# Optimization experiments

Measured on AMD Instinct MI355X. Metric: run time of the kernel, lower is better.

## Reference

```python
import math
import jax, jax.numpy as jnp
import numpy as np

H_CYCLES, L_CYCLES = 3, 2
STD = 0.02


def setup_inputs() -> dict:
    key = jax.random.key(0)
    ks = jax.random.split(key, 11)
    D, nh, mult, V, T, B = 512, 8, 64, 8192, 512, 4
    N = mult * D // nh
    def nrm(k, shape):
        return jax.random.normal(k, shape, jnp.float32) * STD
    return {
        "idx": jax.random.randint(ks[0], (B, T), 0, V),
        "embed_w": nrm(ks[1], (V, D)),
        "h_enc": nrm(ks[2], (nh, D, N)),
        "h_enc_v": nrm(ks[3], (nh, D, N)),
        "h_dec": nrm(ks[4], (nh * N, D)),
        "l_enc": nrm(ks[5], (nh, D, N)),
        "l_enc_v": nrm(ks[6], (nh, D, N)),
        "l_dec": nrm(ks[7], (nh * N, D)),
        "lm_head": nrm(ks[8], (D, V)),
        "h_init": nrm(ks[9], (D,)),
        "l_init": nrm(ks[10], (D,)),
    }


def _ln(x, eps=1e-5):
    # LayerNorm without affine params (elementwise_affine=False)
    m = jnp.mean(x, axis=-1, keepdims=True)
    v = jnp.var(x, axis=-1, keepdims=True)
    return (x - m) * jax.lax.rsqrt(v + eps)


def _rope_tables(T, N):
    # freqs with even-quantized exponent, angles wrapped mod 1 then scaled by 2*pi
    q = jnp.floor(jnp.arange(N, dtype=jnp.float32) / 2.0) * 2.0
    freqs = 1.0 / jnp.power(2.0 ** 16, q / N) / (2.0 * math.pi)
    phases = jnp.arange(T, dtype=jnp.float32)[:, None] * freqs[None, :]
    ang = (phases % 1.0) * (2.0 * math.pi)
    return jnp.cos(ang), jnp.sin(ang)  # each (T, N)


def _rope(v, cos, sin):
    # v: (B, nh, T, N); interleaved rotation as in torch stack/view trick
    v_rot = jnp.stack((-v[..., 1::2], v[..., ::2]), axis=-1).reshape(v.shape)
    return v * cos + v_rot * sin


def _attn(x_sparse, Vmat, cos, sin):
    # x_sparse: (B, nh, T, N); Vmat: (B, T, D)
    N = x_sparse.shape[-1]
    T = x_sparse.shape[-2]
    QR = _rope(x_sparse, cos, sin)
    scores = jnp.einsum('bhtn,bhsn->bhts', QR, QR) * (N ** -0.5)
    mask = jnp.tril(jnp.ones((T, T), dtype=bool), k=-1)  # strict lower triangle
    scores = jnp.where(mask, scores, 0.0)
    return jnp.einsum('bhts,bsd->bhtd', scores, Vmat)  # (B, nh, T, D)


def _block(x, inj, enc, enc_v, dec, cos, sin):
    # x, inj: (B, 1, T, D)
    B, _, T, D = x.shape
    nh, _, N = enc.shape
    xi = _ln(x + inj)[:, 0]  # (B, T, D)
    x_sparse = jax.nn.relu(jnp.einsum('btd,hdn->bhtn', xi, enc))
    yKV = _ln(_attn(x_sparse, xi, cos, sin))  # (B, nh, T, D)
    y_sparse = jax.nn.relu(jnp.einsum('bhtd,hdn->bhtn', yKV, enc_v))
    xy = (x_sparse * y_sparse).transpose(0, 2, 1, 3).reshape(B, 1, T, nh * N)
    y = _ln(xy @ dec)  # (B, 1, T, D)
    return _ln(x + y)


def reference(idx, embed_w, h_enc, h_enc_v, h_dec, l_enc, l_enc_v, l_dec,
              lm_head, h_init, l_init):
    B, T = idx.shape
    D = embed_w.shape[1]
    N = l_enc.shape[-1]
    cos, sin = _rope_tables(T, N)
    inp = _ln(embed_w[idx])[:, None]  # (B, 1, T, D)
    z_H = jnp.broadcast_to(h_init, (B, 1, T, D))
    z_L = jnp.broadcast_to(l_init, (B, 1, T, D))
    for h in range(H_CYCLES):
        for l in range(L_CYCLES):
            if not (h == H_CYCLES - 1 and l == L_CYCLES - 1):
                z_L = _block(z_L, z_H + inp, l_enc, l_enc_v, l_dec, cos, sin)
        if h < H_CYCLES - 1:
            z_H = _block(z_H, z_L, h_enc, h_enc_v, h_dec, cos, sin)
    z_L = _block(z_L, z_H + inp, l_enc, l_enc_v, l_dec, cos, sin)
    z_H = _block(z_H, z_L, h_enc, h_enc_v, h_dec, cos, sin)
    logits = z_H[:, 0] @ lm_head  # (B, T, vocab)
    return logits
```

## Files before the change

### kernel.cpp

```cpp
#include <hip/hip_runtime.h>

typedef _Float16 f16;
typedef __attribute__((ext_vector_type(8))) _Float16 f16x8;
typedef __attribute__((ext_vector_type(4))) float f32x4;
typedef __attribute__((ext_vector_type(4))) int i32x4;

#define D_  512
#define NH_ 8
#define NS_ 4096
#define TT_ 512
#define BB_ 4
#define VV_ 8192
#define HN_ 32768
#define BT_ 2048


__device__ __forceinline__ void gl16(const void* g, void* l) {
  __builtin_amdgcn_global_load_lds((const __attribute__((address_space(1))) void*)g,
                                   (__attribute__((address_space(3))) void*)l, 16, 0, 0);
}

__device__ __forceinline__ void gemm_core(const f16* __restrict__ A, const f16* __restrict__ B,
    int lda, int ldb, int nk, char* As, char* Bs, f32x4 acc[4][4]) {
  int tid = threadIdx.x;
  int l = tid & 63, wid = tid >> 6;
  int wm = wid >> 1, wn = wid & 1;
  int row0 = tid >> 3, g0 = tid & 7;
  for (int kt = 0; kt < nk; ++kt) {
    __syncthreads();
#pragma unroll
    for (int it = 0; it < 4; ++it) {
      int row = row0 + 32 * it;
      int gs = g0 ^ (row & 7);
      int wb = (wid * 64 + it * 256) * 16;
      gl16(A + (size_t)row * lda + gs * 8, As + wb);
      gl16(B + (size_t)row * ldb + gs * 8, Bs + wb);
    }
    __syncthreads();
    A += 64; B += 64;
#pragma unroll
    for (int kh = 0; kh < 2; ++kh) {
      f16x8 af[4], bfr[4];
#pragma unroll
      for (int m = 0; m < 4; ++m) {
        int row = wm * 64 + m * 16 + (l & 15);
        af[m] = *(const f16x8*)(As + row * 128 + ((kh * 64 + (l >> 4) * 16) ^ ((row & 7) << 4)));
      }
#pragma unroll
      for (int n = 0; n < 4; ++n) {
        int row = wn * 64 + n * 16 + (l & 15);
        bfr[n] = *(const f16x8*)(Bs + row * 128 + ((kh * 64 + (l >> 4) * 16) ^ ((row & 7) << 4)));
      }
#pragma unroll
      for (int m = 0; m < 4; ++m)
#pragma unroll
        for (int n = 0; n < 4; ++n)
          acc[m][n] = __builtin_amdgcn_mfma_f32_16x16x32_f16(af[m], bfr[n], acc[m][n], 0, 0, 0);
    }
  }
}


__global__ __launch_bounds__(256, 4) void k_gemm_xs(
    const f16* __restrict__ xi, const f16* __restrict__ encT,
    const f16* __restrict__ csT, f16* __restrict__ qr) {
  __shared__ i32x4 As4[1024], Bs4[1024];
  int bid = blockIdx.x;
  int swz = (bid & 7) * 512 + (bid >> 3);
  int mt = swz & 15, nt = (swz >> 4) & 31, h = swz >> 9;
  const f16* A = xi + (size_t)mt * 128 * D_;
  const f16* B = encT + ((size_t)h * NS_ + nt * 128) * D_;
  f32x4 acc[4][4] = {};
  gemm_core(A, B, D_, D_, D_ / 64, (char*)As4, (char*)Bs4, acc);
  int l = threadIdx.x & 63, wid = threadIdx.x >> 6;
  int wm = wid >> 1, wn = wid & 1;
  int r04 = (l >> 4) * 4, c0 = l & 15;
  int b = (mt * 128) >> 9;
  int tbase = (mt * 128) & (TT_ - 1);
#pragma unroll
  for (int m = 0; m < 4; ++m)
#pragma unroll
    for (int n = 0; n < 4; ++n)
#pragma unroll
      for (int r = 0; r < 4; ++r) {
        int row = wm * 64 + m * 16 + r04 + r;
        int col = wn * 64 + n * 16 + c0;
        int t = tbase + row;
        int nn = nt * 128 + col;
        float xsv = fmaxf(acc[m][n][r], 0.f);
        float prt = __shfl_xor(xsv, 1);
        int ci = 2 * (t * NS_ + nn);
        float c = (float)csT[ci], s = (float)csT[ci + 1];
        float qv = xsv * c + ((nn & 1) ? prt : -prt) * s;
        size_t o = (((size_t)b * NH_ + h) * TT_ + t) * NS_ + nn;
        qr[o] = (f16)qv;
      }
}

__global__ __launch_bounds__(256, 4) void k_gemm_scores(
    const f16* __restrict__ qr, f16* __restrict__ scores) {
  __shared__ i32x4 As4[1024], Bs4[1024];
  int bid = blockIdx.x;
  int swz = (bid & 7) * 40 + (bid >> 3);
  int x = swz % 10, z = swz / 10;
  int mt = (x >= 6) ? 3 : (x >= 3) ? 2 : (x >= 1) ? 1 : 0;
  int nt = x - mt * (mt + 1) / 2;
  const f16* base = qr + (size_t)z * TT_ * NS_;
  const f16* A = base + (size_t)mt * 128 * NS_;
  const f16* B = base + (size_t)nt * 128 * NS_;
  f32x4 acc[4][4] = {};
  gemm_core(A, B, NS_, NS_, NS_ / 64, (char*)As4, (char*)Bs4, acc);
  int l = threadIdx.x & 63, wid = threadIdx.x >> 6;
  int wm = wid >> 1, wn = wid & 1;
  int r04 = (l >> 4) * 4, c0 = l & 15;
  f16* outp = scores + (size_t)z * TT_ * TT_;
#pragma unroll
  for (int m = 0; m < 4; ++m)
#pragma unroll
    for (int n = 0; n < 4; ++n)
#pragma unroll
      for (int r = 0; r < 4; ++r) {
        int t = mt * 128 + wm * 64 + m * 16 + r04 + r;
        int s_ = nt * 128 + wn * 64 + n * 16 + c0;
        float v = (t > s_) ? acc[m][n][r] * 0.015625f : 0.f;
        outp[(size_t)t * TT_ + s_] = (f16)v;
      }
}

__global__ __launch_bounds__(256, 4) void k_gemm_attn(
    const f16* __restrict__ scores, const f16* __restrict__ xiT, f16* __restrict__ attn) {
  __shared__ i32x4 As4[1024], Bs4[1024];
  int bid = blockIdx.x;
  int swz = (bid & 7) * 64 + (bid >> 3);
  int mt = swz & 3, ntd = (swz >> 2) & 3, z = swz >> 4;
  int b = z >> 3;
  const f16* A = scores + (size_t)z * TT_ * TT_ + (size_t)mt * 128 * TT_;
  const f16* B = xiT + (size_t)b * D_ * TT_ + (size_t)ntd * 128 * TT_;
  f32x4 acc[4][4] = {};
  gemm_core(A, B, TT_, TT_, 2 * mt + 2, (char*)As4, (char*)Bs4, acc);
  int l = threadIdx.x & 63, wid = threadIdx.x >> 6;
  int wm = wid >> 1, wn = wid & 1;
  int r04 = (l >> 4) * 4, c0 = l & 15;
#pragma unroll
  for (int m = 0; m < 4; ++m)
#pragma unroll
    for (int n = 0; n < 4; ++n)
#pragma unroll
      for (int r = 0; r < 4; ++r) {
        int t = mt * 128 + wm * 64 + m * 16 + r04 + r;
        int d = ntd * 128 + wn * 64 + n * 16 + c0;
        attn[((size_t)z * TT_ + t) * D_ + d] = (f16)acc[m][n][r];
      }
}

__global__ __launch_bounds__(256, 4) void k_gemm_xy(
    const f16* __restrict__ ykv, const f16* __restrict__ encvT,
    const f16* __restrict__ csT, f16* __restrict__ qrxy) {
  __shared__ i32x4 As4[1024], Bs4[1024];
  int bid = blockIdx.x;
  int swz = (bid & 7) * 512 + (bid >> 3);
  int mt = swz & 3, nt = (swz >> 2) & 31, z = swz >> 7;
  int h = z & 7;
  const f16* A = ykv + (size_t)z * TT_ * D_ + (size_t)mt * 128 * D_;
  const f16* B = encvT + ((size_t)h * NS_ + nt * 128) * D_;
  f32x4 acc[4][4] = {};
  gemm_core(A, B, D_, D_, D_ / 64, (char*)As4, (char*)Bs4, acc);
  int l = threadIdx.x & 63, wid = threadIdx.x >> 6;
  int wm = wid >> 1, wn = wid & 1;
  int r04 = (l >> 4) * 4, c0 = l & 15;
#pragma unroll
  for (int m = 0; m < 4; ++m)
#pragma unroll
    for (int n = 0; n < 4; ++n)
#pragma unroll
      for (int r = 0; r < 4; ++r) {
        int t = mt * 128 + wm * 64 + m * 16 + r04 + r;
        int nn = nt * 128 + wn * 64 + n * 16 + c0;
        float ys = fmaxf(acc[m][n][r], 0.f);
        size_t o = ((size_t)z * TT_ + t) * NS_ + nn;
        float qv = (float)qrxy[o];
        float prt = __shfl_xor(qv, 1);
        int ci = 2 * (t * NS_ + nn);
        float c = (float)csT[ci], s = (float)csT[ci + 1];
        float xsv = (nn & 1) ? (qv * c - prt * s) : (qv * c + prt * s);
        qrxy[o] = (f16)(xsv * ys);
      }
}

__global__ __launch_bounds__(256, 4) void k_gemm_ydec(
    const f16* __restrict__ xy, const f16* __restrict__ decT, f16* __restrict__ ypart) {
  __shared__ i32x4 As4[1024], Bs4[1024];
  int bid = blockIdx.x;
  int swz = (bid & 7) * 64 + (bid >> 3);
  int mt = swz & 15, nt = (swz >> 4) & 3, kz = swz >> 6;
  int b = mt >> 2, t0 = (mt & 3) * 128;
  const f16* A = xy + ((size_t)(b * NH_ + kz) * TT_ + t0) * NS_;
  const f16* B = decT + (size_t)nt * 128 * HN_ + (size_t)kz * NS_;
  f32x4 acc[4][4] = {};
  gemm_core(A, B, NS_, HN_, NS_ / 64, (char*)As4, (char*)Bs4, acc);
  int l = threadIdx.x & 63, wid = threadIdx.x >> 6;
  int wm = wid >> 1, wn = wid & 1;
  int r04 = (l >> 4) * 4, c0 = l & 15;
  f16* outp = ypart + (size_t)kz * BT_ * D_;
#pragma unroll
  for (int m = 0; m < 4; ++m)
#pragma unroll
    for (int n = 0; n < 4; ++n)
#pragma unroll
      for (int r = 0; r < 4; ++r) {
        int R = mt * 128 + wm * 64 + m * 16 + r04 + r;
        int c = nt * 128 + wn * 64 + n * 16 + c0;
        outp[(size_t)R * D_ + c] = (f16)acc[m][n][r];
      }
}

__global__ __launch_bounds__(256, 4) void k_gemm_logits(
    const f16* __restrict__ zbf, const f16* __restrict__ lmT, float* __restrict__ outp) {
  __shared__ i32x4 As4[1024], Bs4[1024];
  int bid = blockIdx.x;
  int swz = (bid & 7) * 128 + (bid >> 3);
  int mt = swz & 15, nt = swz >> 4;
  const f16* A = zbf + (size_t)mt * 128 * D_;
  const f16* B = lmT + (size_t)nt * 128 * D_;
  f32x4 acc[4][4] = {};
  gemm_core(A, B, D_, D_, D_ / 64, (char*)As4, (char*)Bs4, acc);
  int l = threadIdx.x & 63, wid = threadIdx.x >> 6;
  int wm = wid >> 1, wn = wid & 1;
  int r04 = (l >> 4) * 4, c0 = l & 15;
#pragma unroll
  for (int m = 0; m < 4; ++m)
#pragma unroll
    for (int n = 0; n < 4; ++n)
#pragma unroll
      for (int r = 0; r < 4; ++r) {
        int R = mt * 128 + wm * 64 + m * 16 + r04 + r;
        int v = nt * 128 + wn * 64 + n * 16 + c0;
        outp[(size_t)R * VV_ + v] = acc[m][n][r];
      }
}


__device__ __forceinline__ float wave_sum(float v) {
#pragma unroll
  for (int o = 32; o > 0; o >>= 1) v += __shfl_xor(v, o);
  return v;
}

__global__ __launch_bounds__(256) void k_tables(f16* __restrict__ csT) {
  int i = blockIdx.x * 256 + threadIdx.x;
  int t = i >> 12, n = i & (NS_ - 1);
  float q = (float)(n & ~1);
  float freq = exp2f(-16.f * q / 4096.f) * 0.15915494309189535f;
  float ph = (float)t * freq;
  ph -= floorf(ph);
  float ang = ph * 6.283185307179586f;
  csT[2 * i]     = (f16)cosf(ang);
  csT[2 * i + 1] = (f16)sinf(ang);
}

__global__ void k_transpose(const float* __restrict__ in, f16* __restrict__ outp, int R, int C) {
  __shared__ float tile[32][33];
  size_t mo = (size_t)blockIdx.z * R * C;
  in += mo; outp += mo;
  int c0 = blockIdx.x * 32, r0 = blockIdx.y * 32;
#pragma unroll
  for (int i = threadIdx.y; i < 32; i += 8)
    tile[i][threadIdx.x] = in[(size_t)(r0 + i) * C + c0 + threadIdx.x];
  __syncthreads();
#pragma unroll
  for (int i = threadIdx.y; i < 32; i += 8)
    outp[(size_t)(c0 + i) * R + r0 + threadIdx.x] = (f16)tile[threadIdx.x][i];
}

__global__ __launch_bounds__(256) void k_embed_ln(const int* __restrict__ idx,
    const float* __restrict__ emb, f16* __restrict__ inp) {
  int r = blockIdx.x * 4 + (threadIdx.x >> 6);
  int lane = threadIdx.x & 63;
  const float* e = emb + (size_t)idx[r] * D_ + lane * 8;
  f32x4 e0 = *(const f32x4*)e;
  f32x4 e1 = *(const f32x4*)(e + 4);
  float v[8];
#pragma unroll
  for (int i = 0; i < 4; ++i) { v[i] = e0[i]; v[i + 4] = e1[i]; }
  float s = 0.f;
#pragma unroll
  for (int i = 0; i < 8; ++i) s += v[i];
  float mean = wave_sum(s) * (1.f / 512.f);
  float q = 0.f;
#pragma unroll
  for (int i = 0; i < 8; ++i) { v[i] -= mean; q += v[i] * v[i]; }
  float rs = rsqrtf(wave_sum(q) * (1.f / 512.f) + 1e-5f);
  f16x8 ov;
#pragma unroll
  for (int i = 0; i < 8; ++i) ov[i] = (f16)(v[i] * rs);
  *(f16x8*)(inp + (size_t)r * D_ + lane * 8) = ov;
}

__global__ __launch_bounds__(256) void k_init(const float* __restrict__ hi,
    const float* __restrict__ li, f16* __restrict__ zH, f16* __restrict__ zL) {
  size_t i = (size_t)blockIdx.x * 256 + threadIdx.x;
  zH[i] = (f16)hi[i & (D_ - 1)];
  zL[i] = (f16)li[i & (D_ - 1)];
}

__global__ __launch_bounds__(256) void k_ln_xi(const f16* __restrict__ x,
    const f16* __restrict__ a1, const f16* __restrict__ a2,
    f16* __restrict__ xi, f16* __restrict__ xiT) {
  int r = blockIdx.x * 4 + (threadIdx.x >> 6);
  int lane = threadIdx.x & 63;
  size_t o = (size_t)r * D_ + lane * 8;
  f16x8 xv = *(const f16x8*)(x + o);
  f16x8 av = *(const f16x8*)(a1 + o);
  float v[8];
#pragma unroll
  for (int i = 0; i < 8; ++i) v[i] = (float)xv[i] + (float)av[i];
  if (a2) {
    f16x8 bv = *(const f16x8*)(a2 + o);
#pragma unroll
    for (int i = 0; i < 8; ++i) v[i] += (float)bv[i];
  }
  float s = 0.f;
#pragma unroll
  for (int i = 0; i < 8; ++i) s += v[i];
  float mean = wave_sum(s) * (1.f / 512.f);
  float q = 0.f;
#pragma unroll
  for (int i = 0; i < 8; ++i) { v[i] -= mean; q += v[i] * v[i]; }
  float rs = rsqrtf(wave_sum(q) * (1.f / 512.f) + 1e-5f);
  f16x8 ov;
#pragma unroll
  for (int i = 0; i < 8; ++i) ov[i] = (f16)(v[i] * rs);
  *(f16x8*)(xi + o) = ov;
  int b = r >> 9, t = r & (TT_ - 1);
  int d0 = lane * 8;
#pragma unroll
  for (int i = 0; i < 8; ++i)
    xiT[((size_t)b * D_ + d0 + i) * TT_ + t] = ov[i];
}

__global__ __launch_bounds__(256) void k_ln_rows(const f16* __restrict__ in, f16* __restrict__ outp) {
  int r = blockIdx.x * 4 + (threadIdx.x >> 6);
  int lane = threadIdx.x & 63;
  size_t o = (size_t)r * D_ + lane * 8;
  f16x8 xv = *(const f16x8*)(in + o);
  float v[8];
#pragma unroll
  for (int i = 0; i < 8; ++i) v[i] = (float)xv[i];
  float s = 0.f;
#pragma unroll
  for (int i = 0; i < 8; ++i) s += v[i];
  float mean = wave_sum(s) * (1.f / 512.f);
  float q = 0.f;
#pragma unroll
  for (int i = 0; i < 8; ++i) { v[i] -= mean; q += v[i] * v[i]; }
  float rs = rsqrtf(wave_sum(q) * (1.f / 512.f) + 1e-5f);
  f16x8 ov;
#pragma unroll
  for (int i = 0; i < 8; ++i) ov[i] = (f16)(v[i] * rs);
  *(f16x8*)(outp + o) = ov;
}

__global__ __launch_bounds__(256) void k_ln_y_out(const f16* __restrict__ ypart,
    f16* __restrict__ z) {
  int r = blockIdx.x * 4 + (threadIdx.x >> 6);
  int lane = threadIdx.x & 63;
  size_t o = (size_t)r * D_ + lane * 8;
  float v[8] = {};
#pragma unroll
  for (int k = 0; k < 8; ++k) {
    f16x8 p = *(const f16x8*)(ypart + (size_t)k * BT_ * D_ + o);
#pragma unroll
    for (int i = 0; i < 8; ++i) v[i] += (float)p[i];
  }
  float s = 0.f;
#pragma unroll
  for (int i = 0; i < 8; ++i) s += v[i];
  float mean = wave_sum(s) * (1.f / 512.f);
  float q = 0.f;
#pragma unroll
  for (int i = 0; i < 8; ++i) { v[i] -= mean; q += v[i] * v[i]; }
  float rs = rsqrtf(wave_sum(q) * (1.f / 512.f) + 1e-5f);
  f16x8 zv = *(const f16x8*)(z + o);
#pragma unroll
  for (int i = 0; i < 8; ++i) v[i] = (float)zv[i] + v[i] * rs;
  s = 0.f;
#pragma unroll
  for (int i = 0; i < 8; ++i) s += v[i];
  mean = wave_sum(s) * (1.f / 512.f);
  q = 0.f;
#pragma unroll
  for (int i = 0; i < 8; ++i) { v[i] -= mean; q += v[i] * v[i]; }
  rs = rsqrtf(wave_sum(q) * (1.f / 512.f) + 1e-5f);
  f16x8 ov;
#pragma unroll
  for (int i = 0; i < 8; ++i) ov[i] = (f16)(v[i] * rs);
  *(f16x8*)(z + o) = ov;
}


extern "C" void kernel_launch(void* const* d_in, const int* in_sizes, int n_in,
                              void* d_out, int out_size, void* d_ws, size_t ws_size,
                              hipStream_t stream) {
  (void)in_sizes; (void)n_in; (void)out_size;
  const int*   idx    = (const int*)  d_in[0];
  const float* emb    = (const float*)d_in[1];
  const float* h_enc  = (const float*)d_in[2];
  const float* h_encv = (const float*)d_in[3];
  const float* h_dec  = (const float*)d_in[4];
  const float* l_enc  = (const float*)d_in[5];
  const float* l_encv = (const float*)d_in[6];
  const float* l_dec  = (const float*)d_in[7];
  const float* lm     = (const float*)d_in[8];
  const float* h_init = (const float*)d_in[9];
  const float* l_init = (const float*)d_in[10];
  float* out = (float*)d_out;

  bool resident = ws_size >= ((size_t)352 << 20);

  char* w = (char*)d_ws;
  size_t off = 0;
  auto alloc = [&](size_t n) { void* p = w + off; off += (n + 255) & ~(size_t)255; return p; };
  f16* csT = (f16*)alloc(8388608);
  f16 *encT[2], *encvT[2], *decT[2], *lmT;
  if (resident) {
    for (int s = 0; s < 2; ++s) {
      encT[s]  = (f16*)alloc(33554432);
      encvT[s] = (f16*)alloc(33554432);
      decT[s]  = (f16*)alloc(33554432);
    }
    lmT = (f16*)alloc(8388608);
  } else {
    encT[0]  = encT[1]  = (f16*)alloc(33554432);
    encvT[0] = encvT[1] = (f16*)alloc(33554432);
    decT[0]  = decT[1]  = (f16*)alloc(33554432);
    lmT = encT[0];
  }
  f16* inp    = (f16*)alloc(2097152);
  f16* zH     = (f16*)alloc(2097152);
  f16* zL     = (f16*)alloc(2097152);
  f16* xi_bf  = (f16*)alloc(2097152);
  f16* xiT_bf = (f16*)alloc(2097152);
  f16* qrxy   = (f16*)alloc(134217728);

  f16* scoresB = (f16*)d_out;
  f16* attnP   = (f16*)((char*)d_out + 16777216);
  f16* ypart   = attnP;
  f16* ykv     = (f16*)((char*)d_out + 33554432);

  dim3 tb(32, 8);
  auto transpose_set = [&](int sel) {
    const float* e  = sel ? h_enc  : l_enc;
    const float* ev = sel ? h_encv : l_encv;
    const float* dc = sel ? h_dec  : l_dec;
    k_transpose<<<dim3(128, 16, 8), tb, 0, stream>>>(e,  encT[sel],  512, 4096);
    k_transpose<<<dim3(128, 16, 8), tb, 0, stream>>>(ev, encvT[sel], 512, 4096);
    k_transpose<<<dim3(16, 1024, 1), tb, 0, stream>>>(dc, decT[sel], 32768, 512);
  };

  k_tables<<<8192, 256, 0, stream>>>(csT);
  k_embed_ln<<<512, 256, 0, stream>>>(idx, emb, inp);
  k_init<<<4096, 256, 0, stream>>>(h_init, l_init, zH, zL);
  if (resident) {
    transpose_set(0);
    transpose_set(1);
    k_transpose<<<dim3(256, 16, 1), tb, 0, stream>>>(lm, lmT, 512, 8192);
  }

  int cur = -1;
  auto setw = [&](int sel) {
    if (resident || cur == sel) { cur = sel; return; }
    cur = sel;
    transpose_set(sel);
  };

  auto run_block = [&](f16* zx, const f16* a1, const f16* a2, int s) {
    k_ln_xi<<<512, 256, 0, stream>>>(zx, a1, a2, xi_bf, xiT_bf);
    k_gemm_xs<<<4096, 256, 0, stream>>>(xi_bf, encT[s], csT, qrxy);
    k_gemm_scores<<<320, 256, 0, stream>>>(qrxy, scoresB);
    k_gemm_attn<<<512, 256, 0, stream>>>(scoresB, xiT_bf, attnP);
    k_ln_rows<<<4096, 256, 0, stream>>>(attnP, ykv);
    k_gemm_xy<<<4096, 256, 0, stream>>>(ykv, encvT[s], csT, qrxy);
    k_gemm_ydec<<<512, 256, 0, stream>>>(qrxy, decT[s], ypart);
    k_ln_y_out<<<512, 256, 0, stream>>>(ypart, zx);
  };

  for (int i = 0; i < 3; ++i) {
    setw(0);
    run_block(zL, inp, zH, 0);
    run_block(zL, inp, zH, 0);
    setw(1);
    run_block(zH, zL, (const f16*)nullptr, 1);
  }
  if (!resident)
    k_transpose<<<dim3(256, 16, 1), tb, 0, stream>>>(lm, lmT, 512, 8192);
  k_gemm_logits<<<1024, 256, 0, stream>>>(zH, lmT, out);
}
```

Measured before the change: 4.054 ms.

## Double-buffer LDS tiles in the shared GEMM core to overlap loads with MFMA

The shared GEMM main loop now stages the first K tile up front. On each iteration it issues the direct-to-LDS global loads for the next tile into a second buffer while running MFMAs on the current one. This cuts the loop from two barriers per iteration to one, aiming to hide global load latency behind compute. The cost is LDS per block doubling to 64KB, and launch bounds drop from 4 to 2 blocks per CU, which lowers occupancy and the latency hiding that came from running many blocks at once.

```diff
diff --git a/kernel.cpp b/kernel.cpp
--- a/kernel.cpp
+++ b/kernel.cpp
@@ -20,24 +20,35 @@
                                    (__attribute__((address_space(3))) void*)l, 16, 0, 0);
 }
 
+__device__ __forceinline__ void stage_tile(const f16* __restrict__ A, const f16* __restrict__ B,
+                                           int lda, int ldb, char* As, char* Bs) {
+  int tid = threadIdx.x;
+  int row0 = tid >> 3, g0 = tid & 7;
+  int wb0 = (tid >> 6) * 1024;
+#pragma unroll
+  for (int it = 0; it < 4; ++it) {
+    int row = row0 + 32 * it;
+    int gs = g0 ^ (row & 7);
+    gl16(A + (size_t)row * lda + gs * 8, As + wb0 + it * 4096);
+    gl16(B + (size_t)row * ldb + gs * 8, Bs + wb0 + it * 4096);
+  }
+}
+
 __device__ __forceinline__ void gemm_core(const f16* __restrict__ A, const f16* __restrict__ B,
-    int lda, int ldb, int nk, char* As, char* Bs, f32x4 acc[4][4]) {
+    int lda, int ldb, int nk, char* sh, f32x4 acc[4][4]) {
   int tid = threadIdx.x;
   int l = tid & 63, wid = tid >> 6;
   int wm = wid >> 1, wn = wid & 1;
-  int row0 = tid >> 3, g0 = tid & 7;
+  stage_tile(A, B, lda, ldb, sh, sh + 16384);
+  __syncthreads();
   for (int kt = 0; kt < nk; ++kt) {
-    __syncthreads();
-#pragma unroll
-    for (int it = 0; it < 4; ++it) {
-      int row = row0 + 32 * it;
-      int gs = g0 ^ (row & 7);
-      int wb = (wid * 64 + it * 256) * 16;
-      gl16(A + (size_t)row * lda + gs * 8, As + wb);
-      gl16(B + (size_t)row * ldb + gs * 8, Bs + wb);
-    }
-    __syncthreads();
-    A += 64; B += 64;
+    int cur = (kt & 1) * 32768;
+    int nxt = cur ^ 32768;
+    if (kt + 1 < nk)
+      stage_tile(A + (size_t)(kt + 1) * 64, B + (size_t)(kt + 1) * 64, lda, ldb,
+                 sh + nxt, sh + nxt + 16384);
+    const char* As = sh + cur;
+    const char* Bs = sh + cur + 16384;
 #pragma unroll
     for (int kh = 0; kh < 2; ++kh) {
       f16x8 af[4], bfr[4];
@@ -57,21 +68,22 @@
         for (int n = 0; n < 4; ++n)
           acc[m][n] = __builtin_amdgcn_mfma_f32_16x16x32_f16(af[m], bfr[n], acc[m][n], 0, 0, 0);
     }
-  }
-}
-
-
-__global__ __launch_bounds__(256, 4) void k_gemm_xs(
+    __syncthreads();
+  }
+}
+
+
+__global__ __launch_bounds__(256, 2) void k_gemm_xs(
     const f16* __restrict__ xi, const f16* __restrict__ encT,
     const f16* __restrict__ csT, f16* __restrict__ qr) {
-  __shared__ i32x4 As4[1024], Bs4[1024];
+  __shared__ char sh[65536];
   int bid = blockIdx.x;
   int swz = (bid & 7) * 512 + (bid >> 3);
   int mt = swz & 15, nt = (swz >> 4) & 31, h = swz >> 9;
   const f16* A = xi + (size_t)mt * 128 * D_;
   const f16* B = encT + ((size_t)h * NS_ + nt * 128) * D_;
   f32x4 acc[4][4] = {};
-  gemm_core(A, B, D_, D_, D_ / 64, (char*)As4, (char*)Bs4, acc);
+  gemm_core(A, B, D_, D_, D_ / 64, sh, acc);
   int l = threadIdx.x & 63, wid = threadIdx.x >> 6;
   int wm = wid >> 1, wn = wid & 1;
   int r04 = (l >> 4) * 4, c0 = l & 15;
@@ -97,9 +109,9 @@
       }
 }
 
-__global__ __launch_bounds__(256, 4) void k_gemm_scores(
+__global__ __launch_bounds__(256, 2) void k_gemm_scores(
     const f16* __restrict__ qr, f16* __restrict__ scores) {
-  __shared__ i32x4 As4[1024], Bs4[1024];
+  __shared__ char sh[65536];
   int bid = blockIdx.x;
   int swz = (bid & 7) * 40 + (bid >> 3);
   int x = swz % 10, z = swz / 10;
@@ -109,7 +121,7 @@
   const f16* A = base + (size_t)mt * 128 * NS_;
   const f16* B = base + (size_t)nt * 128 * NS_;
   f32x4 acc[4][4] = {};
-  gemm_core(A, B, NS_, NS_, NS_ / 64, (char*)As4, (char*)Bs4, acc);
+  gemm_core(A, B, NS_, NS_, NS_ / 64, sh, acc);
   int l = threadIdx.x & 63, wid = threadIdx.x >> 6;
   int wm = wid >> 1, wn = wid & 1;
   int r04 = (l >> 4) * 4, c0 = l & 15;
@@ -127,9 +139,9 @@
       }
 }
 
-__global__ __launch_bounds__(256, 4) void k_gemm_attn(
+__global__ __launch_bounds__(256, 2) void k_gemm_attn(
     const f16* __restrict__ scores, const f16* __restrict__ xiT, f16* __restrict__ attn) {
-  __shared__ i32x4 As4[1024], Bs4[1024];
+  __shared__ char sh[65536];
   int bid = blockIdx.x;
   int swz = (bid & 7) * 64 + (bid >> 3);
   int mt = swz & 3, ntd = (swz >> 2) & 3, z = swz >> 4;
@@ -137,7 +149,7 @@
   const f16* A = scores + (size_t)z * TT_ * TT_ + (size_t)mt * 128 * TT_;
   const f16* B = xiT + (size_t)b * D_ * TT_ + (size_t)ntd * 128 * TT_;
   f32x4 acc[4][4] = {};
-  gemm_core(A, B, TT_, TT_, 2 * mt + 2, (char*)As4, (char*)Bs4, acc);
+  gemm_core(A, B, TT_, TT_, 2 * mt + 2, sh, acc);
   int l = threadIdx.x & 63, wid = threadIdx.x >> 6;
   int wm = wid >> 1, wn = wid & 1;
   int r04 = (l >> 4) * 4, c0 = l & 15;
@@ -153,10 +165,10 @@
       }
 }
 
-__global__ __launch_bounds__(256, 4) void k_gemm_xy(
+__global__ __launch_bounds__(256, 2) void k_gemm_xy(
     const f16* __restrict__ ykv, const f16* __restrict__ encvT,
     const f16* __restrict__ csT, f16* __restrict__ qrxy) {
-  __shared__ i32x4 As4[1024], Bs4[1024];
+  __shared__ char sh[65536];
   int bid = blockIdx.x;
   int swz = (bid & 7) * 512 + (bid >> 3);
   int mt = swz & 3, nt = (swz >> 2) & 31, z = swz >> 7;
@@ -164,7 +176,7 @@
   const f16* A = ykv + (size_t)z * TT_ * D_ + (size_t)mt * 128 * D_;
   const f16* B = encvT + ((size_t)h * NS_ + nt * 128) * D_;
   f32x4 acc[4][4] = {};
-  gemm_core(A, B, D_, D_, D_ / 64, (char*)As4, (char*)Bs4, acc);
+  gemm_core(A, B, D_, D_, D_ / 64, sh, acc);
   int l = threadIdx.x & 63, wid = threadIdx.x >> 6;
   int wm = wid >> 1, wn = wid & 1;
   int r04 = (l >> 4) * 4, c0 = l & 15;
@@ -187,9 +199,9 @@
       }
 }
 
-__global__ __launch_bounds__(256, 4) void k_gemm_ydec(
+__global__ __launch_bounds__(256, 2) void k_gemm_ydec(
     const f16* __restrict__ xy, const f16* __restrict__ decT, f16* __restrict__ ypart) {
-  __shared__ i32x4 As4[1024], Bs4[1024];
+  __shared__ char sh[65536];
   int bid = blockIdx.x;
   int swz = (bid & 7) * 64 + (bid >> 3);
   int mt = swz & 15, nt = (swz >> 4) & 3, kz = swz >> 6;
@@ -197,7 +209,7 @@
   const f16* A = xy + ((size_t)(b * NH_ + kz) * TT_ + t0) * NS_;
   const f16* B = decT + (size_t)nt * 128 * HN_ + (size_t)kz * NS_;
   f32x4 acc[4][4] = {};
-  gemm_core(A, B, NS_, HN_, NS_ / 64, (char*)As4, (char*)Bs4, acc);
+  gemm_core(A, B, NS_, HN_, NS_ / 64, sh, acc);
   int l = threadIdx.x & 63, wid = threadIdx.x >> 6;
   int wm = wid >> 1, wn = wid & 1;
   int r04 = (l >> 4) * 4, c0 = l & 15;
@@ -214,16 +226,16 @@
       }
 }
 
-__global__ __launch_bounds__(256, 4) void k_gemm_logits(
+__global__ __launch_bounds__(256, 2) void k_gemm_logits(
     const f16* __restrict__ zbf, const f16* __restrict__ lmT, float* __restrict__ outp) {
-  __shared__ i32x4 As4[1024], Bs4[1024];
+  __shared__ char sh[65536];
   int bid = blockIdx.x;
   int swz = (bid & 7) * 128 + (bid >> 3);
   int mt = swz & 15, nt = swz >> 4;
   const f16* A = zbf + (size_t)mt * 128 * D_;
   const f16* B = lmT + (size_t)nt * 128 * D_;
   f32x4 acc[4][4] = {};
-  gemm_core(A, B, D_, D_, D_ / 64, (char*)As4, (char*)Bs4, acc);
+  gemm_core(A, B, D_, D_, D_ / 64, sh, acc);
   int l = threadIdx.x & 63, wid = threadIdx.x >> 6;
   int wm = wid >> 1, wn = wid & 1;
   int r04 = (l >> 4) * 4, c0 = l & 15;
```

Result: no change. 4.117 ms (+1.6%).

## Widen GEMM tiles to 128x256 with 8-wave blocks and XCD-aware mapping

Applied to the files above, without the earlier changes.

Adds a gemm_core_w variant that runs 512-thread blocks (8 waves, 2x4) computing 128x256 output tiles, and switches the xs, xy, ydec and logits GEMMs to it with half the grid size. Each A tile loaded into LDS is now reused across twice as many columns, which cuts global and LDS traffic per FLOP. Block-to-tile mapping is also rewritten so that blocks sharing a head or N-range land on the same XCD. In exchange, LDS per block grows to 48KB and the grid shrinks, which lowers occupancy. The ydec kernel drops to 256 blocks, which may underfill the GPU.

```diff
diff --git a/kernel.cpp b/kernel.cpp
--- a/kernel.cpp
+++ b/kernel.cpp
@@ -60,23 +60,66 @@
   }
 }
 
-
-__global__ __launch_bounds__(256, 4) void k_gemm_xs(
+__device__ __forceinline__ void gemm_core_w(const f16* __restrict__ A, const f16* __restrict__ B,
+    int lda, int ldb, int nk, char* As, char* Bs, f32x4 acc[4][4]) {
+  int tid = threadIdx.x;
+  int l = tid & 63, wid = tid >> 6;
+  int wm = wid >> 2, wn = wid & 3;
+  int row0 = tid >> 3, g0 = tid & 7;
+  for (int kt = 0; kt < nk; ++kt) {
+    __syncthreads();
+#pragma unroll
+    for (int it = 0; it < 2; ++it) {
+      int row = row0 + 64 * it;
+      int gs = g0 ^ (row & 7);
+      gl16(A + (size_t)row * lda + gs * 8, As + (wid * 64 + it * 512) * 16);
+    }
+#pragma unroll
+    for (int it = 0; it < 4; ++it) {
+      int row = row0 + 64 * it;
+      int gs = g0 ^ (row & 7);
+      gl16(B + (size_t)row * ldb + gs * 8, Bs + (wid * 64 + it * 512) * 16);
+    }
+    __syncthreads();
+    A += 64; B += 64;
+#pragma unroll
+    for (int kh = 0; kh < 2; ++kh) {
+      f16x8 af[4], bfr[4];
+#pragma unroll
+      for (int m = 0; m < 4; ++m) {
+        int row = wm * 64 + m * 16 + (l & 15);
+        af[m] = *(const f16x8*)(As + row * 128 + ((kh * 64 + (l >> 4) * 16) ^ ((row & 7) << 4)));
+      }
+#pragma unroll
+      for (int n = 0; n < 4; ++n) {
+        int row = wn * 64 + n * 16 + (l & 15);
+        bfr[n] = *(const f16x8*)(Bs + row * 128 + ((kh * 64 + (l >> 4) * 16) ^ ((row & 7) << 4)));
+      }
+#pragma unroll
+      for (int m = 0; m < 4; ++m)
+#pragma unroll
+        for (int n = 0; n < 4; ++n)
+          acc[m][n] = __builtin_amdgcn_mfma_f32_16x16x32_f16(af[m], bfr[n], acc[m][n], 0, 0, 0);
+    }
+  }
+}
+
+
+__global__ __launch_bounds__(512, 4) void k_gemm_xs(
     const f16* __restrict__ xi, const f16* __restrict__ encT,
     const f16* __restrict__ csT, f16* __restrict__ qr) {
-  __shared__ i32x4 As4[1024], Bs4[1024];
+  __shared__ char sh[49152];
   int bid = blockIdx.x;
-  int swz = (bid & 7) * 512 + (bid >> 3);
-  int mt = swz & 15, nt = (swz >> 4) & 31, h = swz >> 9;
+  int h = bid & 7, k = bid >> 3;
+  int nt = k >> 4, mt = k & 15;
   const f16* A = xi + (size_t)mt * 128 * D_;
-  const f16* B = encT + ((size_t)h * NS_ + nt * 128) * D_;
+  const f16* B = encT + ((size_t)h * NS_ + nt * 256) * D_;
   f32x4 acc[4][4] = {};
-  gemm_core(A, B, D_, D_, D_ / 64, (char*)As4, (char*)Bs4, acc);
+  gemm_core_w(A, B, D_, D_, D_ / 64, sh, sh + 16384, acc);
   int l = threadIdx.x & 63, wid = threadIdx.x >> 6;
-  int wm = wid >> 1, wn = wid & 1;
+  int wm = wid >> 2, wn = wid & 3;
   int r04 = (l >> 4) * 4, c0 = l & 15;
-  int b = (mt * 128) >> 9;
-  int tbase = (mt * 128) & (TT_ - 1);
+  int b = mt >> 2, tbase = (mt & 3) * 128;
 #pragma unroll
   for (int m = 0; m < 4; ++m)
 #pragma unroll
@@ -86,7 +129,7 @@
         int row = wm * 64 + m * 16 + r04 + r;
         int col = wn * 64 + n * 16 + c0;
         int t = tbase + row;
-        int nn = nt * 128 + col;
+        int nn = nt * 256 + col;
         float xsv = fmaxf(acc[m][n][r], 0.f);
         float prt = __shfl_xor(xsv, 1);
         int ci = 2 * (t * NS_ + nn);
@@ -153,20 +196,20 @@
       }
 }
 
-__global__ __launch_bounds__(256, 4) void k_gemm_xy(
+__global__ __launch_bounds__(512, 4) void k_gemm_xy(
     const f16* __restrict__ ykv, const f16* __restrict__ encvT,
     const f16* __restrict__ csT, f16* __restrict__ qrxy) {
-  __shared__ i32x4 As4[1024], Bs4[1024];
+  __shared__ char sh[49152];
   int bid = blockIdx.x;
-  int swz = (bid & 7) * 512 + (bid >> 3);
-  int mt = swz & 3, nt = (swz >> 2) & 31, z = swz >> 7;
-  int h = z & 7;
+  int h = bid & 7, k = bid >> 3;
+  int b = k >> 6, nt = (k >> 2) & 15, mt = k & 3;
+  int z = b * NH_ + h;
   const f16* A = ykv + (size_t)z * TT_ * D_ + (size_t)mt * 128 * D_;
-  const f16* B = encvT + ((size_t)h * NS_ + nt * 128) * D_;
+  const f16* B = encvT + ((size_t)h * NS_ + nt * 256) * D_;
   f32x4 acc[4][4] = {};
-  gemm_core(A, B, D_, D_, D_ / 64, (char*)As4, (char*)Bs4, acc);
+  gemm_core_w(A, B, D_, D_, D_ / 64, sh, sh + 16384, acc);
   int l = threadIdx.x & 63, wid = threadIdx.x >> 6;
-  int wm = wid >> 1, wn = wid & 1;
+  int wm = wid >> 2, wn = wid & 3;
   int r04 = (l >> 4) * 4, c0 = l & 15;
 #pragma unroll
   for (int m = 0; m < 4; ++m)
@@ -175,7 +218,7 @@
 #pragma unroll
       for (int r = 0; r < 4; ++r) {
         int t = mt * 128 + wm * 64 + m * 16 + r04 + r;
-        int nn = nt * 128 + wn * 64 + n * 16 + c0;
+        int nn = nt * 256 + wn * 64 + n * 16 + c0;
         float ys = fmaxf(acc[m][n][r], 0.f);
         size_t o = ((size_t)z * TT_ + t) * NS_ + nn;
         float qv = (float)qrxy[o];
@@ -187,19 +230,19 @@
       }
 }
 
-__global__ __launch_bounds__(256, 4) void k_gemm_ydec(
+__global__ __launch_bounds__(512, 4) void k_gemm_ydec(
     const f16* __restrict__ xy, const f16* __restrict__ decT, f16* __restrict__ ypart) {
-  __shared__ i32x4 As4[1024], Bs4[1024];
+  __shared__ char sh[49152];
   int bid = blockIdx.x;
-  int swz = (bid & 7) * 64 + (bid >> 3);
-  int mt = swz & 15, nt = (swz >> 4) & 3, kz = swz >> 6;
+  int kz = bid & 7, k = bid >> 3;
+  int mt = k >> 1, nt = k & 1;
   int b = mt >> 2, t0 = (mt & 3) * 128;
   const f16* A = xy + ((size_t)(b * NH_ + kz) * TT_ + t0) * NS_;
-  const f16* B = decT + (size_t)nt * 128 * HN_ + (size_t)kz * NS_;
+  const f16* B = decT + (size_t)nt * 256 * HN_ + (size_t)kz * NS_;
   f32x4 acc[4][4] = {};
-  gemm_core(A, B, NS_, HN_, NS_ / 64, (char*)As4, (char*)Bs4, acc);
+  gemm_core_w(A, B, NS_, HN_, NS_ / 64, sh, sh + 16384, acc);
   int l = threadIdx.x & 63, wid = threadIdx.x >> 6;
-  int wm = wid >> 1, wn = wid & 1;
+  int wm = wid >> 2, wn = wid & 3;
   int r04 = (l >> 4) * 4, c0 = l & 15;
   f16* outp = ypart + (size_t)kz * BT_ * D_;
 #pragma unroll
@@ -209,23 +252,23 @@
 #pragma unroll
       for (int r = 0; r < 4; ++r) {
         int R = mt * 128 + wm * 64 + m * 16 + r04 + r;
-        int c = nt * 128 + wn * 64 + n * 16 + c0;
+        int c = nt * 256 + wn * 64 + n * 16 + c0;
         outp[(size_t)R * D_ + c] = (f16)acc[m][n][r];
       }
 }
 
-__global__ __launch_bounds__(256, 4) void k_gemm_logits(
+__global__ __launch_bounds__(512, 4) void k_gemm_logits(
     const f16* __restrict__ zbf, const f16* __restrict__ lmT, float* __restrict__ outp) {
-  __shared__ i32x4 As4[1024], Bs4[1024];
+  __shared__ char sh[49152];
   int bid = blockIdx.x;
-  int swz = (bid & 7) * 128 + (bid >> 3);
-  int mt = swz & 15, nt = swz >> 4;
+  int xcd = bid & 7, k = bid >> 3;
+  int nt = xcd * 4 + (k >> 4), mt = k & 15;
   const f16* A = zbf + (size_t)mt * 128 * D_;
-  const f16* B = lmT + (size_t)nt * 128 * D_;
+  const f16* B = lmT + (size_t)nt * 256 * D_;
   f32x4 acc[4][4] = {};
-  gemm_core(A, B, D_, D_, D_ / 64, (char*)As4, (char*)Bs4, acc);
+  gemm_core_w(A, B, D_, D_, D_ / 64, sh, sh + 16384, acc);
   int l = threadIdx.x & 63, wid = threadIdx.x >> 6;
-  int wm = wid >> 1, wn = wid & 1;
+  int wm = wid >> 2, wn = wid & 3;
   int r04 = (l >> 4) * 4, c0 = l & 15;
 #pragma unroll
   for (int m = 0; m < 4; ++m)
@@ -234,7 +277,7 @@
 #pragma unroll
       for (int r = 0; r < 4; ++r) {
         int R = mt * 128 + wm * 64 + m * 16 + r04 + r;
-        int v = nt * 128 + wn * 64 + n * 16 + c0;
+        int v = nt * 256 + wn * 64 + n * 16 + c0;
         outp[(size_t)R * VV_ + v] = acc[m][n][r];
       }
 }
@@ -475,12 +518,12 @@
 
   auto run_block = [&](f16* zx, const f16* a1, const f16* a2, int s) {
     k_ln_xi<<<512, 256, 0, stream>>>(zx, a1, a2, xi_bf, xiT_bf);
-    k_gemm_xs<<<4096, 256, 0, stream>>>(xi_bf, encT[s], csT, qrxy);
+    k_gemm_xs<<<2048, 512, 0, stream>>>(xi_bf, encT[s], csT, qrxy);
     k_gemm_scores<<<320, 256, 0, stream>>>(qrxy, scoresB);
     k_gemm_attn<<<512, 256, 0, stream>>>(scoresB, xiT_bf, attnP);
     k_ln_rows<<<4096, 256, 0, stream>>>(attnP, ykv);
-    k_gemm_xy<<<4096, 256, 0, stream>>>(ykv, encvT[s], csT, qrxy);
-    k_gemm_ydec<<<512, 256, 0, stream>>>(qrxy, decT[s], ypart);
+    k_gemm_xy<<<2048, 512, 0, stream>>>(ykv, encvT[s], csT, qrxy);
+    k_gemm_ydec<<<256, 512, 0, stream>>>(qrxy, decT[s], ypart);
     k_ln_y_out<<<512, 256, 0, stream>>>(ypart, zx);
   };
 
@@ -493,5 +536,5 @@
   }
   if (!resident)
     k_transpose<<<dim3(256, 16, 1), tb, 0, stream>>>(lm, lmT, 512, 8192);
-  k_gemm_logits<<<1024, 256, 0, stream>>>(zH, lmT, out);
-}
+  k_gemm_logits<<<512, 512, 0, stream>>>(zH, lmT, out);
+}
```

Measured after the change: 4.375 ms. 1.08x slower.

## Split-K the scores and y-decoder GEMMs to fill more CUs

Applied to the files above, without the earlier changes.

The causal scores GEMM now splits its 4096-long K dimension into two halves. Each half writes fp32 partial tiles, and a new reduce kernel sums them, applies the scale and causal mask, and converts to f16. The y-decoder GEMM likewise splits each head's K range in two, producing 16 partial outputs that the LayerNorm epilogue kernel sums. This doubles the grid sizes (320→640 and 512→1024 blocks) to improve load balance across CUs, at the cost of extra partial-sum memory traffic and one extra kernel launch per block.

```diff
diff --git a/kernel.cpp b/kernel.cpp
--- a/kernel.cpp
+++ b/kernel.cpp
@@ -97,34 +97,62 @@
       }
 }
 
-__global__ __launch_bounds__(256, 4) void k_gemm_scores(
-    const f16* __restrict__ qr, f16* __restrict__ scores) {
+__global__ __launch_bounds__(256, 4) void k_gemm_scores_part(
+    const f16* __restrict__ qr, float* __restrict__ pscore) {
   __shared__ i32x4 As4[1024], Bs4[1024];
   int bid = blockIdx.x;
-  int swz = (bid & 7) * 40 + (bid >> 3);
-  int x = swz % 10, z = swz / 10;
+  int idx = (bid & 7) * 80 + (bid >> 3);
+  int half = idx & 1, tileT = idx >> 1;
+  int x = tileT % 10, z = tileT / 10;
   int mt = (x >= 6) ? 3 : (x >= 3) ? 2 : (x >= 1) ? 1 : 0;
   int nt = x - mt * (mt + 1) / 2;
-  const f16* base = qr + (size_t)z * TT_ * NS_;
+  const f16* base = qr + (size_t)z * TT_ * NS_ + half * 2048;
   const f16* A = base + (size_t)mt * 128 * NS_;
   const f16* B = base + (size_t)nt * 128 * NS_;
   f32x4 acc[4][4] = {};
-  gemm_core(A, B, NS_, NS_, NS_ / 64, (char*)As4, (char*)Bs4, acc);
+  gemm_core(A, B, NS_, NS_, 32, (char*)As4, (char*)Bs4, acc);
   int l = threadIdx.x & 63, wid = threadIdx.x >> 6;
   int wm = wid >> 1, wn = wid & 1;
   int r04 = (l >> 4) * 4, c0 = l & 15;
+  float* outp = pscore + (size_t)(half * 320 + tileT) * 16384;
+#pragma unroll
+  for (int m = 0; m < 4; ++m)
+#pragma unroll
+    for (int n = 0; n < 4; ++n)
+#pragma unroll
+      for (int r = 0; r < 4; ++r) {
+        int tl = wm * 64 + m * 16 + r04 + r;
+        int sl = wn * 64 + n * 16 + c0;
+        outp[tl * 128 + sl] = acc[m][n][r];
+      }
+}
+
+__global__ __launch_bounds__(256) void k_scores_reduce(
+    const float* __restrict__ pscore, f16* __restrict__ scores) {
+  int T = blockIdx.x;
+  int x = T % 10, z = T / 10;
+  int mt = (x >= 6) ? 3 : (x >= 3) ? 2 : (x >= 1) ? 1 : 0;
+  int nt = x - mt * (mt + 1) / 2;
+  const float* p0 = pscore + (size_t)T * 16384;
+  const float* p1 = pscore + (size_t)(320 + T) * 16384;
   f16* outp = scores + (size_t)z * TT_ * TT_;
 #pragma unroll
-  for (int m = 0; m < 4; ++m)
-#pragma unroll
-    for (int n = 0; n < 4; ++n)
-#pragma unroll
-      for (int r = 0; r < 4; ++r) {
-        int t = mt * 128 + wm * 64 + m * 16 + r04 + r;
-        int s_ = nt * 128 + wn * 64 + n * 16 + c0;
-        float v = (t > s_) ? acc[m][n][r] * 0.015625f : 0.f;
-        outp[(size_t)t * TT_ + s_] = (f16)v;
-      }
+  for (int j = 0; j < 8; ++j) {
+    int i = threadIdx.x * 64 + j * 8;
+    int t = mt * 128 + (i >> 7);
+    int s0 = nt * 128 + (i & 127);
+    f32x4 a0 = *(const f32x4*)(p0 + i);
+    f32x4 a1 = *(const f32x4*)(p0 + i + 4);
+    f32x4 b0 = *(const f32x4*)(p1 + i);
+    f32x4 b1 = *(const f32x4*)(p1 + i + 4);
+    f16x8 q;
+#pragma unroll
+    for (int e = 0; e < 4; ++e) {
+      q[e]     = (f16)((t > s0 + e)     ? (a0[e] + b0[e]) * 0.015625f : 0.f);
+      q[e + 4] = (f16)((t > s0 + e + 4) ? (a1[e] + b1[e]) * 0.015625f : 0.f);
+    }
+    *(f16x8*)(outp + (size_t)t * TT_ + s0 + (i >> 7) * 0) = q;
+  }
 }
 
 __global__ __launch_bounds__(256, 4) void k_gemm_attn(
@@ -191,17 +219,17 @@
     const f16* __restrict__ xy, const f16* __restrict__ decT, f16* __restrict__ ypart) {
   __shared__ i32x4 As4[1024], Bs4[1024];
   int bid = blockIdx.x;
-  int swz = (bid & 7) * 64 + (bid >> 3);
-  int mt = swz & 15, nt = (swz >> 4) & 3, kz = swz >> 6;
+  int h = bid & 7, k = bid >> 3;
+  int half = k & 1, mt = (k >> 1) & 15, nt = k >> 5;
   int b = mt >> 2, t0 = (mt & 3) * 128;
-  const f16* A = xy + ((size_t)(b * NH_ + kz) * TT_ + t0) * NS_;
-  const f16* B = decT + (size_t)nt * 128 * HN_ + (size_t)kz * NS_;
+  const f16* A = xy + ((size_t)(b * NH_ + h) * TT_ + t0) * NS_ + half * 2048;
+  const f16* B = decT + (size_t)nt * 128 * HN_ + (size_t)h * NS_ + half * 2048;
   f32x4 acc[4][4] = {};
-  gemm_core(A, B, NS_, HN_, NS_ / 64, (char*)As4, (char*)Bs4, acc);
+  gemm_core(A, B, NS_, HN_, 32, (char*)As4, (char*)Bs4, acc);
   int l = threadIdx.x & 63, wid = threadIdx.x >> 6;
   int wm = wid >> 1, wn = wid & 1;
   int r04 = (l >> 4) * 4, c0 = l & 15;
-  f16* outp = ypart + (size_t)kz * BT_ * D_;
+  f16* outp = ypart + (size_t)(h * 2 + half) * BT_ * D_;
 #pragma unroll
   for (int m = 0; m < 4; ++m)
 #pragma unroll
@@ -367,7 +395,7 @@
   size_t o = (size_t)r * D_ + lane * 8;
   float v[8] = {};
 #pragma unroll
-  for (int k = 0; k < 8; ++k) {
+  for (int k = 0; k < 16; ++k) {
     f16x8 p = *(const f16x8*)(ypart + (size_t)k * BT_ * D_ + o);
 #pragma unroll
     for (int i = 0; i < 8; ++i) v[i] += (float)p[i];
@@ -442,10 +470,11 @@
   f16* xiT_bf = (f16*)alloc(2097152);
   f16* qrxy   = (f16*)alloc(134217728);
 
-  f16* scoresB = (f16*)d_out;
-  f16* attnP   = (f16*)((char*)d_out + 16777216);
-  f16* ypart   = attnP;
-  f16* ykv     = (f16*)((char*)d_out + 33554432);
+  f16*   scoresB = (f16*)d_out;
+  float* pscore  = (float*)((char*)d_out + 16777216);
+  f16*   attnP   = (f16*)((char*)d_out + 16777216);
+  f16*   ypart   = attnP;
+  f16*   ykv     = (f16*)((char*)d_out + 33554432);
 
   dim3 tb(32, 8);
   auto transpose_set = [&](int sel) {
@@ -476,11 +505,12 @@
   auto run_block = [&](f16* zx, const f16* a1, const f16* a2, int s) {
     k_ln_xi<<<512, 256, 0, stream>>>(zx, a1, a2, xi_bf, xiT_bf);
     k_gemm_xs<<<4096, 256, 0, stream>>>(xi_bf, encT[s], csT, qrxy);
-    k_gemm_scores<<<320, 256, 0, stream>>>(qrxy, scoresB);
+    k_gemm_scores_part<<<640, 256, 0, stream>>>(qrxy, pscore);
+    k_scores_reduce<<<320, 256, 0, stream>>>(pscore, scoresB);
     k_gemm_attn<<<512, 256, 0, stream>>>(scoresB, xiT_bf, attnP);
     k_ln_rows<<<4096, 256, 0, stream>>>(attnP, ykv);
     k_gemm_xy<<<4096, 256, 0, stream>>>(ykv, encvT[s], csT, qrxy);
-    k_gemm_ydec<<<512, 256, 0, stream>>>(qrxy, decT[s], ypart);
+    k_gemm_ydec<<<1024, 256, 0, stream>>>(qrxy, decT[s], ypart);
     k_ln_y_out<<<512, 256, 0, stream>>>(ypart, zx);
   };
 
```

After: 4.189 ms. 3.3% more time.
